# Kernel tuning notes

Hardware: AMD Instinct MI355X
Metric: run time of the kernel (lower is better)

Reference implementation:

```python
import jax, jax.numpy as jnp
import numpy as np

K = 5        # kernel_size per pseudo-dim
DIM = 2      # pseudo-coordinate dimensionality
K2 = K * K   # total kernel weight matrices
N_NODES = 50000


def spline_basis(edge_attr):
    """Open B-spline basis, degree=1, dim=2. Returns basis [E,4], weight_index [E,4]."""
    v = edge_attr * (K - 1)                      # [E,2], pseudo in [0,1]
    lo = jnp.floor(v)
    frac = v - lo                                # [E,2]
    lo = lo.astype(jnp.int32)
    fac = jnp.stack([1.0 - frac, frac], axis=-1)                 # [E,2,2] (dim, bit)
    idx = jnp.clip(lo[..., None] + jnp.arange(2), 0, K - 1)      # [E,2,2]
    b0 = jnp.array([0, 1, 0, 1])  # bit for dim 0, per spline term
    b1 = jnp.array([0, 0, 1, 1])  # bit for dim 1
    basis = fac[:, 0, b0] * fac[:, 1, b1]        # [E,4]
    wi = idx[:, 0, b0] * K + idx[:, 1, b1]       # [E,4] flat kernel index
    return basis, wi


def spline_conv(x, src, dst, basis, wi, W, root, bias, n_nodes):
    """SplineConv with mean aggregation, root weight and bias.
    x:[N,Fin] W:[K2,Fin,Fout] root:[Fin,Fout] bias:[Fout]"""
    E = src.shape[0]
    K2_, Fin, Fout = W.shape
    # scatter the 4 sparse basis values into a dense per-edge kernel-coeff matrix [E,K2]
    coeff = jnp.zeros((E, K2_), x.dtype).at[jnp.arange(E)[:, None], wi].add(basis)
    xj = x[src]                                  # gather source features [E,Fin]
    msg = jnp.zeros((E, Fout), x.dtype)
    for k in range(K2_):                         # fixed small loop over 25 kernels
        msg = msg + coeff[:, k:k + 1] * (xj @ W[k])
    agg = jax.ops.segment_sum(msg, dst, num_segments=n_nodes)    # [N,Fout]
    deg = jax.ops.segment_sum(jnp.ones((E,), x.dtype), dst, num_segments=n_nodes)
    agg = agg / jnp.clip(deg, 1.0)[:, None]      # mean aggregation
    return agg + x @ root + bias


def setup_inputs() -> dict:
    key = jax.random.key(0)
    ks = jax.random.split(key, 9)
    E = 800000
    Fin, H, C = 64, 16, 7
    x = jax.random.normal(ks[0], (N_NODES, Fin), dtype=jnp.float32)
    edge_index = jax.random.randint(ks[1], (2, E), 0, N_NODES, dtype=jnp.int64)
    edge_attr = jax.random.uniform(ks[2], (E, DIM), dtype=jnp.float32)
    s1 = 1.0 / np.sqrt(Fin)
    s2 = 1.0 / np.sqrt(H)
    W1 = jax.random.uniform(ks[3], (K2, Fin, H), jnp.float32, -s1, s1)
    root1 = jax.random.uniform(ks[4], (Fin, H), jnp.float32, -s1, s1)
    bias1 = jax.random.uniform(ks[5], (H,), jnp.float32, -s1, s1)
    W2 = jax.random.uniform(ks[6], (K2, H, C), jnp.float32, -s2, s2)
    root2 = jax.random.uniform(ks[7], (H, C), jnp.float32, -s2, s2)
    bias2 = jax.random.uniform(ks[8], (C,), jnp.float32, -s2, s2)
    return {"x": x, "edge_index": edge_index, "edge_attr": edge_attr,
            "W1": W1, "root1": root1, "bias1": bias1,
            "W2": W2, "root2": root2, "bias2": bias2}


def reference(x, edge_index, edge_attr, W1, root1, bias1, W2, root2, bias2):
    src = edge_index[0]
    dst = edge_index[1]
    basis, wi = spline_basis(edge_attr)
    h = jax.nn.relu(spline_conv(x, src, dst, basis, wi, W1, root1, bias1, N_NODES))
    # dropout(p=0.6) is identity in eval mode
    out = spline_conv(h, src, dst, basis, wi, W2, root2, bias2, N_NODES)
    return jax.nn.log_softmax(out, axis=1)
```

## Files before the change

### kernel.cpp

```cpp
#include <hip/hip_runtime.h>

#define KK2 25
#define FIN 64
#define HH 16
#define CC 7
#define KSPLIT 5

#define SCAN_VPT 4
#define SCAN_BLK 256
#define SCAN_CHUNK (SCAN_VPT * SCAN_BLK)

__device__ inline unsigned short f2bf(float f) {
    unsigned u = __float_as_uint(f);
    return (unsigned short)((u + 0x7FFFu + ((u >> 16) & 1u)) >> 16);
}
__device__ inline float bf2f(unsigned short b) {
    return __uint_as_float(((unsigned)b) << 16);
}

__global__ void k_hist(const int* __restrict__ ei, int* __restrict__ cnt, int E) {
    int e = blockIdx.x * 256 + threadIdx.x;
    if (e < E) atomicAdd(&cnt[ei[E + e]], 1);
}

__global__ void k_bsum(const int* __restrict__ cnt, int* __restrict__ bsum, int N) {
    int b = blockIdx.x, t = threadIdx.x;
    int base = b * SCAN_CHUNK + t * SCAN_VPT;
    int s = 0;
#pragma unroll
    for (int j = 0; j < SCAN_VPT; j++) {
        int i = base + j;
        if (i < N) s += cnt[i];
    }
#pragma unroll
    for (int d = 1; d < 64; d <<= 1) s += __shfl_xor(s, d, 64);
    __shared__ int sd[SCAN_BLK / 64];
    if ((t & 63) == 0) sd[t >> 6] = s;
    __syncthreads();
    if (t == 0) {
        int tot = 0;
        for (int w = 0; w < SCAN_BLK / 64; w++) tot += sd[w];
        bsum[b] = tot;
    }
}

__global__ void k_bscan(const int* __restrict__ bsum, int* __restrict__ boff, int nblk) {
    int t = threadIdx.x;
    __shared__ int sd[256];
    int v = (t < nblk) ? bsum[t] : 0;
    sd[t] = v;
    __syncthreads();
    for (int off = 1; off < 256; off <<= 1) {
        int u = (t >= off) ? sd[t - off] : 0;
        __syncthreads();
        sd[t] += u;
        __syncthreads();
    }
    boff[t] = sd[t] - v;
}

__global__ void k_sfin(const int* __restrict__ cnt, const int* __restrict__ boff,
                       int* __restrict__ rowStart, int* __restrict__ cursor, int N) {
    int b = blockIdx.x, t = threadIdx.x;
    int base = b * SCAN_CHUNK + t * SCAN_VPT;
    int v[SCAN_VPT];
    int s = 0;
#pragma unroll
    for (int j = 0; j < SCAN_VPT; j++) {
        int i = base + j;
        v[j] = (i < N) ? cnt[i] : 0;
        s += v[j];
    }
    __shared__ int sd[SCAN_BLK];
    sd[t] = s;
    __syncthreads();
    for (int off = 1; off < SCAN_BLK; off <<= 1) {
        int u = (t >= off) ? sd[t - off] : 0;
        __syncthreads();
        sd[t] += u;
        __syncthreads();
    }
    int run = sd[t] - s + boff[b];
#pragma unroll
    for (int j = 0; j < SCAN_VPT; j++) {
        int i = base + j;
        if (i < N) {
            rowStart[i] = run;
            cursor[i] = run;
            run += v[j];
            if (i == N - 1) rowStart[N] = run;
        }
    }
}

__global__ void k_scatter(const float* __restrict__ attr, const int* __restrict__ ei,
                          int* __restrict__ cursor, uint4* __restrict__ rec, int E) {
    int e = blockIdx.x * 256 + threadIdx.x;
    if (e >= E) return;
    float v0 = attr[2 * e] * 4.0f, v1 = attr[2 * e + 1] * 4.0f;
    float l0 = floorf(v0), l1 = floorf(v1);
    float f0 = v0 - l0, f1 = v1 - l1;
    int i0 = (int)l0, i1 = (int)l1;
    int i0a = min(max(i0, 0), 4), i0b = min(max(i0 + 1, 0), 4);
    int i1a = min(max(i1, 0), 4), i1b = min(max(i1 + 1, 0), 4);
    float bx = (1.0f - f0) * (1.0f - f1);
    float by = f0 * (1.0f - f1);
    float bz = (1.0f - f0) * f1;
    float bw = f0 * f1;
    unsigned pack = (unsigned)(i0a * 5 + i1a) | ((unsigned)(i0b * 5 + i1a) << 8) |
                    ((unsigned)(i0a * 5 + i1b) << 16) | ((unsigned)(i0b * 5 + i1b) << 24);
    int s = ei[e], d = ei[E + e];
    int pos = atomicAdd(&cursor[d], 1);
    uint4 r;
    r.x = (unsigned)f2bf(bx) | ((unsigned)f2bf(by) << 16);
    r.y = (unsigned)f2bf(bz) | ((unsigned)f2bf(bw) << 16);
    r.z = (unsigned)s;
    r.w = pack;
    rec[pos] = r;
}

__global__ void k_prepW(const float* __restrict__ W1, const float* __restrict__ W2,
                        float* __restrict__ B1t, float* __restrict__ W2p) {
    int tid = blockIdx.x * 256 + threadIdx.x;
    if (tid < KK2 * FIN * HH) {
        int c = tid >> 6, i = tid & 63;
        int k = c >> 4, h = c & 15;
        B1t[tid] = W1[(k * FIN + i) * HH + h];
    }
    if (tid < KK2 * HH * CC) {
        int k = tid / (HH * CC), r = tid % (HH * CC);
        int i = r / CC, c = r % CC;
        W2p[(k * HH + i) * 8 + c] = W2[tid];
    }
}

__global__ void k_y1(const float* __restrict__ x, const float* __restrict__ B1t,
                     unsigned short* __restrict__ y1Tb, int N, int nbl) {
    __shared__ uint4 sh[4][144];
    int kg = blockIdx.x / nbl;
    int nwin = blockIdx.x % nbl;
    int n = nwin * 256 + threadIdx.x;
    int wv = threadIdx.x >> 6, lane = threadIdx.x & 63;
    bool active = (n < N);
    float4 xr[16];
    if (active) {
        const float4* xp = (const float4*)(x + (size_t)n * 64);
#pragma unroll
        for (int i = 0; i < 16; i++) xr[i] = xp[i];
    }
    int nwb = nwin * 256 + wv * 64;
    int valid = min(64, max(0, N - nwb)) * 2;

    for (int dk = 0; dk < KSPLIT; dk++) {
        int k = kg * KSPLIT + dk;
        const float* B = B1t + k * 16 * 64;
        unsigned tmp[8];
        if (active) {
#pragma unroll
            for (int h4 = 0; h4 < 4; h4++) {
                float a0 = 0, a1 = 0, a2 = 0, a3 = 0;
                const float4* b0 = (const float4*)(B + (h4 * 4 + 0) * 64);
                const float4* b1 = (const float4*)(B + (h4 * 4 + 1) * 64);
                const float4* b2 = (const float4*)(B + (h4 * 4 + 2) * 64);
                const float4* b3 = (const float4*)(B + (h4 * 4 + 3) * 64);
#pragma unroll
                for (int i = 0; i < 16; i++) {
                    float4 xi = xr[i];
                    float4 v0 = b0[i], v1 = b1[i], v2 = b2[i], v3 = b3[i];
                    a0 += xi.x * v0.x + xi.y * v0.y + xi.z * v0.z + xi.w * v0.w;
                    a1 += xi.x * v1.x + xi.y * v1.y + xi.z * v1.z + xi.w * v1.w;
                    a2 += xi.x * v2.x + xi.y * v2.y + xi.z * v2.z + xi.w * v2.w;
                    a3 += xi.x * v3.x + xi.y * v3.y + xi.z * v3.z + xi.w * v3.w;
                }
                tmp[h4 * 2 + 0] = (unsigned)f2bf(a0) | ((unsigned)f2bf(a1) << 16);
                tmp[h4 * 2 + 1] = (unsigned)f2bf(a2) | ((unsigned)f2bf(a3) << 16);
            }
        } else {
#pragma unroll
            for (int j = 0; j < 8; j++) tmp[j] = 0;
        }
        int i0 = lane * 2, i1 = lane * 2 + 1;
        sh[wv][i0 + (i0 >> 3)] = make_uint4(tmp[0], tmp[1], tmp[2], tmp[3]);
        sh[wv][i1 + (i1 >> 3)] = make_uint4(tmp[4], tmp[5], tmp[6], tmp[7]);
        __syncthreads();
        uint4* gbase = (uint4*)(y1Tb + ((size_t)k * N + nwb) * 16);
        int j0 = lane, j1 = lane + 64;
        if (j0 < valid) gbase[j0] = sh[wv][j0 + (j0 >> 3)];
        if (j1 < valid) gbase[j1] = sh[wv][j1 + (j1 >> 3)];
        __syncthreads();
    }
}

__global__ void k_agg1(const int* __restrict__ rowStart, const uint4* __restrict__ rec,
                       const unsigned short* __restrict__ y1Tb, float* __restrict__ agg1,
                       int N) {
    int n = blockIdx.x * 4 + (threadIdx.x >> 6);
    if (n >= N) return;
    int lane = threadIdx.x & 63;
    int sub = lane >> 4, h = lane & 15;
    int start = rowStart[n], end = rowStart[n + 1];
    float acc = 0.0f;
    size_t NN = (size_t)N;
    for (int i = start + sub; i < end; i += 4) {
        uint4 r = rec[i];
        float bx = bf2f((unsigned short)(r.x & 0xffffu));
        float by = bf2f((unsigned short)(r.x >> 16));
        float bz = bf2f((unsigned short)(r.y & 0xffffu));
        float bw = bf2f((unsigned short)(r.y >> 16));
        int s = (int)r.z;
        unsigned w = r.w;
        acc += bx * bf2f(y1Tb[((w & 255u) * NN + s) * 16 + h]);
        acc += by * bf2f(y1Tb[(((w >> 8) & 255u) * NN + s) * 16 + h]);
        acc += bz * bf2f(y1Tb[(((w >> 16) & 255u) * NN + s) * 16 + h]);
        acc += bw * bf2f(y1Tb[((w >> 24) * NN + s) * 16 + h]);
    }
    acc += __shfl_xor(acc, 16, 64);
    acc += __shfl_xor(acc, 32, 64);
    if (lane < 16) agg1[(size_t)n * 16 + h] = acc;
}

__global__ void k_upd1(const float* __restrict__ x, const float* __restrict__ agg1,
                       const int* __restrict__ rowStart, const float* __restrict__ root1,
                       const float* __restrict__ bias1, const float* __restrict__ W2p,
                       float* __restrict__ h1, unsigned short* __restrict__ y2Tb, int N) {
    int n = blockIdx.x * 256 + threadIdx.x;
    if (n >= N) return;
    float inv = 1.0f / (float)max(rowStart[n + 1] - rowStart[n], 1);
    float r[16];
#pragma unroll
    for (int h = 0; h < 16; h++) r[h] = agg1[(size_t)n * 16 + h] * inv + bias1[h];
    const float* xrow = x + (size_t)n * 64;
    for (int i = 0; i < 64; i++) {
        float xi = xrow[i];
        const float* rr = root1 + i * 16;
#pragma unroll
        for (int h = 0; h < 16; h++) r[h] += xi * rr[h];
    }
#pragma unroll
    for (int h = 0; h < 16; h++) r[h] = fmaxf(r[h], 0.0f);
    float4* ho = (float4*)(h1 + (size_t)n * 16);
#pragma unroll
    for (int j = 0; j < 4; j++) ho[j] = make_float4(r[4*j], r[4*j+1], r[4*j+2], r[4*j+3]);
    for (int k = 0; k < 25; k++) {
        float z[8] = {0, 0, 0, 0, 0, 0, 0, 0};
        const float4* wp = (const float4*)(W2p + k * 128);
#pragma unroll
        for (int i = 0; i < 16; i++) {
            float hi = r[i];
            float4 lo = wp[2 * i], hv = wp[2 * i + 1];
            z[0] += hi * lo.x; z[1] += hi * lo.y; z[2] += hi * lo.z; z[3] += hi * lo.w;
            z[4] += hi * hv.x; z[5] += hi * hv.y; z[6] += hi * hv.z; z[7] += hi * hv.w;
        }
        uint4 p;
        p.x = (unsigned)f2bf(z[0]) | ((unsigned)f2bf(z[1]) << 16);
        p.y = (unsigned)f2bf(z[2]) | ((unsigned)f2bf(z[3]) << 16);
        p.z = (unsigned)f2bf(z[4]) | ((unsigned)f2bf(z[5]) << 16);
        p.w = (unsigned)f2bf(z[6]) | ((unsigned)f2bf(z[7]) << 16);
        *(uint4*)(y2Tb + ((size_t)k * N + n) * 8) = p;
    }
}

__global__ void k_agg2(const int* __restrict__ rowStart, const uint4* __restrict__ rec,
                       const unsigned short* __restrict__ y2Tb, float* __restrict__ agg2,
                       int N) {
    int n = blockIdx.x * 4 + (threadIdx.x >> 6);
    if (n >= N) return;
    int lane = threadIdx.x & 63;
    int sub = lane >> 3, c = lane & 7;
    int start = rowStart[n], end = rowStart[n + 1];
    float acc = 0.0f;
    size_t NN = (size_t)N;
    for (int i = start + sub; i < end; i += 8) {
        uint4 r = rec[i];
        float bx = bf2f((unsigned short)(r.x & 0xffffu));
        float by = bf2f((unsigned short)(r.x >> 16));
        float bz = bf2f((unsigned short)(r.y & 0xffffu));
        float bw = bf2f((unsigned short)(r.y >> 16));
        int s = (int)r.z;
        unsigned w = r.w;
        acc += bx * bf2f(y2Tb[((w & 255u) * NN + s) * 8 + c]);
        acc += by * bf2f(y2Tb[(((w >> 8) & 255u) * NN + s) * 8 + c]);
        acc += bz * bf2f(y2Tb[(((w >> 16) & 255u) * NN + s) * 8 + c]);
        acc += bw * bf2f(y2Tb[((w >> 24) * NN + s) * 8 + c]);
    }
    acc += __shfl_xor(acc, 8, 64);
    acc += __shfl_xor(acc, 16, 64);
    acc += __shfl_xor(acc, 32, 64);
    if (lane < 8) agg2[(size_t)n * 8 + c] = acc;
}

__global__ void k_fin2(const float* __restrict__ h1, const float* __restrict__ agg2,
                       const int* __restrict__ rowStart, const float* __restrict__ root2,
                       const float* __restrict__ bias2, float* __restrict__ out, int N) {
    int n = blockIdx.x * 256 + threadIdx.x;
    if (n >= N) return;
    float inv = 1.0f / (float)max(rowStart[n + 1] - rowStart[n], 1);
    float z[7];
#pragma unroll
    for (int c = 0; c < 7; c++) z[c] = agg2[(size_t)n * 8 + c] * inv + bias2[c];
    const float* hrow = h1 + (size_t)n * 16;
#pragma unroll
    for (int i = 0; i < 16; i++) {
        float hi = hrow[i];
        const float* rr = root2 + i * 7;
#pragma unroll
        for (int c = 0; c < 7; c++) z[c] += hi * rr[c];
    }
    float m = z[0];
#pragma unroll
    for (int c = 1; c < 7; c++) m = fmaxf(m, z[c]);
    float ssum = 0.0f;
#pragma unroll
    for (int c = 0; c < 7; c++) ssum += expf(z[c] - m);
    float ls = logf(ssum);
    float* orow = out + (size_t)n * 7;
#pragma unroll
    for (int c = 0; c < 7; c++) orow[c] = z[c] - m - ls;
}

extern "C" void kernel_launch(void* const* d_in, const int* in_sizes, int n_in,
                              void* d_out, int out_size, void* d_ws, size_t ws_size,
                              hipStream_t stream) {
    const float* x     = (const float*)d_in[0];
    const int*   ei    = (const int*)d_in[1];
    const float* attr  = (const float*)d_in[2];
    const float* W1    = (const float*)d_in[3];
    const float* root1 = (const float*)d_in[4];
    const float* bias1 = (const float*)d_in[5];
    const float* W2    = (const float*)d_in[6];
    const float* root2 = (const float*)d_in[7];
    const float* bias2 = (const float*)d_in[8];
    float* out = (float*)d_out;

    int N = in_sizes[0] / FIN;
    int E = in_sizes[1] / 2;

    char* w = (char*)d_ws;
    size_t off = 0;
    auto alloc = [&](size_t bytes) -> void* {
        void* p = w + off;
        off += (bytes + 255) & ~(size_t)255;
        return p;
    };
    int*      cnt      = (int*)alloc((size_t)N * 4);
    int*      rowStart = (int*)alloc((size_t)(N + 1) * 4);
    int*      cursor   = (int*)alloc((size_t)N * 4);
    int*      bsum     = (int*)alloc(260 * 4);
    int*      boff     = (int*)alloc(260 * 4);
    uint4*    rec      = (uint4*)alloc((size_t)E * 16);
    float*    agg1     = (float*)alloc((size_t)N * 64);
    float*    h1       = (float*)alloc((size_t)N * 64);
    float*    agg2     = (float*)alloc((size_t)N * 32);
    float*    B1t      = (float*)alloc((size_t)KK2 * FIN * HH * 4);
    float*    W2p      = (float*)alloc((size_t)KK2 * HH * 8 * 4);
    unsigned short* y1Tb = (unsigned short*)alloc((size_t)N * 400 * 2);
    unsigned short* y2Tb = y1Tb;
    (void)ws_size; (void)n_in; (void)out_size;

    hipMemsetAsync(cnt, 0, (size_t)N * 4, stream);

    int ebl = (E + 255) / 256;
    int nbl = (N + 255) / 256;
    int sblk = (N + SCAN_CHUNK - 1) / SCAN_CHUNK;

    k_hist<<<ebl, 256, 0, stream>>>(ei, cnt, E);
    k_bsum<<<sblk, SCAN_BLK, 0, stream>>>(cnt, bsum, N);
    k_bscan<<<1, 256, 0, stream>>>(bsum, boff, sblk);
    k_sfin<<<sblk, SCAN_BLK, 0, stream>>>(cnt, boff, rowStart, cursor, N);
    k_scatter<<<ebl, 256, 0, stream>>>(attr, ei, cursor, rec, E);
    k_prepW<<<(KK2 * FIN * HH + 255) / 256, 256, 0, stream>>>(W1, W2, B1t, W2p);
    k_y1<<<KSPLIT * nbl, 256, 0, stream>>>(x, B1t, y1Tb, N, nbl);
    k_agg1<<<(N + 3) / 4, 256, 0, stream>>>(rowStart, rec, y1Tb, agg1, N);
    k_upd1<<<nbl, 256, 0, stream>>>(x, agg1, rowStart, root1, bias1, W2p, h1, y2Tb, N);
    k_agg2<<<(N + 3) / 4, 256, 0, stream>>>(rowStart, rec, y2Tb, agg2, N);
    k_fin2<<<nbl, 256, 0, stream>>>(h1, agg2, rowStart, root2, bias2, out, N);
}
```

Before: 306.8 us.

## Fuse node updates into aggregation kernels and split layer-2 projection by kernel group

New measurement: 296.6 us. -3.3%, faster.

```diff
diff --git a/kernel.cpp b/kernel.cpp
--- a/kernel.cpp
+++ b/kernel.cpp
@@ -127,10 +127,10 @@
         int k = c >> 4, h = c & 15;
         B1t[tid] = W1[(k * FIN + i) * HH + h];
     }
-    if (tid < KK2 * HH * CC) {
-        int k = tid / (HH * CC), r = tid % (HH * CC);
-        int i = r / CC, c = r % CC;
-        W2p[(k * HH + i) * 8 + c] = W2[tid];
+    if (tid < KK2 * HH * 8) {
+        int k = tid >> 7, r = tid & 127;
+        int i = r >> 3, c = r & 7;
+        W2p[tid] = (c < CC) ? W2[(k * HH + i) * CC + c] : 0.0f;
     }
 }
 
@@ -191,9 +191,10 @@
     }
 }
 
-__global__ void k_agg1(const int* __restrict__ rowStart, const uint4* __restrict__ rec,
-                       const unsigned short* __restrict__ y1Tb, float* __restrict__ agg1,
-                       int N) {
+__global__ void k_agg1u(const int* __restrict__ rowStart, const uint4* __restrict__ rec,
+                        const unsigned short* __restrict__ y1Tb, const float* __restrict__ x,
+                        const float* __restrict__ root1, const float* __restrict__ bias1,
+                        float* __restrict__ h1, int N) {
     int n = blockIdx.x * 4 + (threadIdx.x >> 6);
     if (n >= N) return;
     int lane = threadIdx.x & 63;
@@ -216,37 +217,36 @@
     }
     acc += __shfl_xor(acc, 16, 64);
     acc += __shfl_xor(acc, 32, 64);
-    if (lane < 16) agg1[(size_t)n * 16 + h] = acc;
-}
-
-__global__ void k_upd1(const float* __restrict__ x, const float* __restrict__ agg1,
-                       const int* __restrict__ rowStart, const float* __restrict__ root1,
-                       const float* __restrict__ bias1, const float* __restrict__ W2p,
-                       float* __restrict__ h1, unsigned short* __restrict__ y2Tb, int N) {
-    int n = blockIdx.x * 256 + threadIdx.x;
+    float inv = 1.0f / (float)max(end - start, 1);
+    float rv = acc * inv + bias1[h];
+    const float* xrow = x + (size_t)n * 64;
+#pragma unroll 8
+    for (int i = 0; i < 64; i++) rv += xrow[i] * root1[i * 16 + h];
+    rv = fmaxf(rv, 0.0f);
+    if (lane < 16) h1[(size_t)n * 16 + h] = rv;
+}
+
+__global__ void k_y2(const float* __restrict__ h1, const float* __restrict__ W2p,
+                     unsigned short* __restrict__ y2Tb, int N, int nbl) {
+    int kg = blockIdx.x / nbl;
+    int n = (blockIdx.x % nbl) * 256 + threadIdx.x;
     if (n >= N) return;
-    float inv = 1.0f / (float)max(rowStart[n + 1] - rowStart[n], 1);
-    float r[16];
-#pragma unroll
-    for (int h = 0; h < 16; h++) r[h] = agg1[(size_t)n * 16 + h] * inv + bias1[h];
-    const float* xrow = x + (size_t)n * 64;
-    for (int i = 0; i < 64; i++) {
-        float xi = xrow[i];
-        const float* rr = root1 + i * 16;
-#pragma unroll
-        for (int h = 0; h < 16; h++) r[h] += xi * rr[h];
-    }
-#pragma unroll
-    for (int h = 0; h < 16; h++) r[h] = fmaxf(r[h], 0.0f);
-    float4* ho = (float4*)(h1 + (size_t)n * 16);
-#pragma unroll
-    for (int j = 0; j < 4; j++) ho[j] = make_float4(r[4*j], r[4*j+1], r[4*j+2], r[4*j+3]);
-    for (int k = 0; k < 25; k++) {
+    float hreg[16];
+    const float4* hp = (const float4*)(h1 + (size_t)n * 16);
+#pragma unroll
+    for (int j = 0; j < 4; j++) {
+        float4 v = hp[j];
+        hreg[4 * j] = v.x; hreg[4 * j + 1] = v.y;
+        hreg[4 * j + 2] = v.z; hreg[4 * j + 3] = v.w;
+    }
+#pragma unroll
+    for (int dk = 0; dk < KSPLIT; dk++) {
+        int k = kg * KSPLIT + dk;
         float z[8] = {0, 0, 0, 0, 0, 0, 0, 0};
         const float4* wp = (const float4*)(W2p + k * 128);
 #pragma unroll
         for (int i = 0; i < 16; i++) {
-            float hi = r[i];
+            float hi = hreg[i];
             float4 lo = wp[2 * i], hv = wp[2 * i + 1];
             z[0] += hi * lo.x; z[1] += hi * lo.y; z[2] += hi * lo.z; z[3] += hi * lo.w;
             z[4] += hi * hv.x; z[5] += hi * hv.y; z[6] += hi * hv.z; z[7] += hi * hv.w;
@@ -260,9 +260,10 @@
     }
 }
 
-__global__ void k_agg2(const int* __restrict__ rowStart, const uint4* __restrict__ rec,
-                       const unsigned short* __restrict__ y2Tb, float* __restrict__ agg2,
-                       int N) {
+__global__ void k_agg2f(const int* __restrict__ rowStart, const uint4* __restrict__ rec,
+                        const unsigned short* __restrict__ y2Tb, const float* __restrict__ h1,
+                        const float* __restrict__ root2, const float* __restrict__ bias2,
+                        float* __restrict__ out, int N) {
     int n = blockIdx.x * 4 + (threadIdx.x >> 6);
     if (n >= N) return;
     int lane = threadIdx.x & 63;
@@ -286,36 +287,27 @@
     acc += __shfl_xor(acc, 8, 64);
     acc += __shfl_xor(acc, 16, 64);
     acc += __shfl_xor(acc, 32, 64);
-    if (lane < 8) agg2[(size_t)n * 8 + c] = acc;
-}
-
-__global__ void k_fin2(const float* __restrict__ h1, const float* __restrict__ agg2,
-                       const int* __restrict__ rowStart, const float* __restrict__ root2,
-                       const float* __restrict__ bias2, float* __restrict__ out, int N) {
-    int n = blockIdx.x * 256 + threadIdx.x;
-    if (n >= N) return;
-    float inv = 1.0f / (float)max(rowStart[n + 1] - rowStart[n], 1);
-    float z[7];
-#pragma unroll
-    for (int c = 0; c < 7; c++) z[c] = agg2[(size_t)n * 8 + c] * inv + bias2[c];
-    const float* hrow = h1 + (size_t)n * 16;
-#pragma unroll
-    for (int i = 0; i < 16; i++) {
-        float hi = hrow[i];
-        const float* rr = root2 + i * 7;
-#pragma unroll
-        for (int c = 0; c < 7; c++) z[c] += hi * rr[c];
-    }
-    float m = z[0];
-#pragma unroll
-    for (int c = 1; c < 7; c++) m = fmaxf(m, z[c]);
-    float ssum = 0.0f;
-#pragma unroll
-    for (int c = 0; c < 7; c++) ssum += expf(z[c] - m);
+    float inv = 1.0f / (float)max(end - start, 1);
+    float z;
+    if (c < CC) {
+        z = acc * inv + bias2[c];
+        const float* hrow = h1 + (size_t)n * 16;
+#pragma unroll
+        for (int i = 0; i < 16; i++) z += hrow[i] * root2[i * CC + c];
+    } else {
+        z = -1e30f;
+    }
+    float m = z;
+    m = fmaxf(m, __shfl_xor(m, 1, 64));
+    m = fmaxf(m, __shfl_xor(m, 2, 64));
+    m = fmaxf(m, __shfl_xor(m, 4, 64));
+    float ex = (c < CC) ? expf(z - m) : 0.0f;
+    float ssum = ex;
+    ssum += __shfl_xor(ssum, 1, 64);
+    ssum += __shfl_xor(ssum, 2, 64);
+    ssum += __shfl_xor(ssum, 4, 64);
     float ls = logf(ssum);
-    float* orow = out + (size_t)n * 7;
-#pragma unroll
-    for (int c = 0; c < 7; c++) orow[c] = z[c] - m - ls;
+    if (lane < CC) out[(size_t)n * 7 + c] = z - m - ls;
 }
 
 extern "C" void kernel_launch(void* const* d_in, const int* in_sizes, int n_in,
@@ -348,9 +340,7 @@
     int*      bsum     = (int*)alloc(260 * 4);
     int*      boff     = (int*)alloc(260 * 4);
     uint4*    rec      = (uint4*)alloc((size_t)E * 16);
-    float*    agg1     = (float*)alloc((size_t)N * 64);
     float*    h1       = (float*)alloc((size_t)N * 64);
-    float*    agg2     = (float*)alloc((size_t)N * 32);
     float*    B1t      = (float*)alloc((size_t)KK2 * FIN * HH * 4);
     float*    W2p      = (float*)alloc((size_t)KK2 * HH * 8 * 4);
     unsigned short* y1Tb = (unsigned short*)alloc((size_t)N * 400 * 2);
@@ -370,8 +360,7 @@
     k_scatter<<<ebl, 256, 0, stream>>>(attr, ei, cursor, rec, E);
     k_prepW<<<(KK2 * FIN * HH + 255) / 256, 256, 0, stream>>>(W1, W2, B1t, W2p);
     k_y1<<<KSPLIT * nbl, 256, 0, stream>>>(x, B1t, y1Tb, N, nbl);
-    k_agg1<<<(N + 3) / 4, 256, 0, stream>>>(rowStart, rec, y1Tb, agg1, N);
-    k_upd1<<<nbl, 256, 0, stream>>>(x, agg1, rowStart, root1, bias1, W2p, h1, y2Tb, N);
-    k_agg2<<<(N + 3) / 4, 256, 0, stream>>>(rowStart, rec, y2Tb, agg2, N);
-    k_fin2<<<nbl, 256, 0, stream>>>(h1, agg2, rowStart, root2, bias2, out, N);
-}
+    k_agg1u<<<(N + 3) / 4, 256, 0, stream>>>(rowStart, rec, y1Tb, x, root1, bias1, h1, N);
+    k_y2<<<KSPLIT * nbl, 256, 0, stream>>>(h1, W2p, y2Tb, N, nbl);
+    k_agg2f<<<(N + 3) / 4, 256, 0, stream>>>(rowStart, rec, y2Tb, h1, root2, bias2, out, N);
+}
```
